# Optimization experiments

Measured on AMD Instinct MI355X. Metric: run time of the kernel, lower is better.

## Reference

```python
import jax, jax.numpy as jnp
import numpy as np

B, S, D, H = 2, 2048, 1024, 16
HD = D // H  # head_dim = 64

def setup_inputs() -> dict:
    key = jax.random.key(0)
    ks = jax.random.split(key, 5)
    scale = 1.0 / np.sqrt(D)
    x = jax.random.normal(ks[0], (B, S, D), dtype=jnp.float32)
    Wq = jax.random.normal(ks[1], (D, D), dtype=jnp.float32) * scale
    Wk = jax.random.normal(ks[2], (D, D), dtype=jnp.float32) * scale
    Wv = jax.random.normal(ks[3], (D, D), dtype=jnp.float32) * scale
    Wf = jax.random.normal(ks[4], (D, D), dtype=jnp.float32) * scale
    z = jnp.zeros((D,), dtype=jnp.float32)
    return {"x": x, "Wq": Wq, "bq": z, "Wk": Wk, "bk": z, "Wv": Wv, "bv": z, "Wf": Wf, "bf": z}

def reference(x, Wq, bq, Wk, bk, Wv, bv, Wf, bf):
    # Linear layers follow torch convention: y = x @ W.T + b
    def split_heads(t):  # [B,S,D] -> [B,H,S,HD]
        return t.reshape(B, S, H, HD).transpose(0, 2, 1, 3)
    q = split_heads(x @ Wq.T + bq)
    k = split_heads(x @ Wk.T + bk)
    v = split_heads(x @ Wv.T + bv)
    scores = jnp.einsum('bhqd,bhkd->bhqk', q, k) / jnp.sqrt(jnp.float32(HD))
    causal = jnp.tril(jnp.ones((S, S), dtype=bool))  # [S,S]
    scores = jnp.where(causal[None, None], scores, -jnp.inf)
    attn = jax.nn.softmax(scores, axis=-1)
    out = jnp.einsum('bhqk,bhkd->bhqd', attn, v)
    out = out.transpose(0, 2, 1, 3).reshape(B, S, D)
    return out @ Wf.T + bf
```

## Files before the change

kernel.cpp:

```cpp
#include <hip/hip_runtime.h>
#include <stdint.h>

#define B_  2
#define S_  2048
#define D_  1024
#define H_  16
#define HD_ 64
#define M_  (B_*S_)

typedef __bf16 bf16x8 __attribute__((ext_vector_type(8)));
typedef float  f32x4  __attribute__((ext_vector_type(4)));

typedef const __attribute__((address_space(1))) void* gas_ptr;
typedef __attribute__((address_space(3))) void* las_ptr;

__device__ __forceinline__ uint16_t f32_to_bf16(float f) {
  uint32_t u = __float_as_uint(f);
  u += 0x7FFFu + ((u >> 16) & 1u);
  return (uint16_t)(u >> 16);
}

__device__ __forceinline__ void g2l16(const uint16_t* g, uint16_t* l) {
  __builtin_amdgcn_global_load_lds((gas_ptr)g, (las_ptr)l, 16, 0, 0);
}

__device__ __forceinline__ int swz_src(int s) {
  return (s >> 2) * D_ + (((s & 3) ^ ((s >> 3) & 3)) * 8);
}

__global__ void cast_all(const float* __restrict__ x,
                         const float* __restrict__ wq, const float* __restrict__ wk,
                         const float* __restrict__ wv, const float* __restrict__ wf,
                         uint16_t* __restrict__ xb,
                         uint16_t* __restrict__ wqb, uint16_t* __restrict__ wkb,
                         uint16_t* __restrict__ wvb, uint16_t* __restrict__ wfb) {
  const int X4 = M_ * D_ / 4;
  const int W4 = D_ * D_ / 4;
  int i = blockIdx.x * 256 + threadIdx.x;
  const float* src; uint16_t* dst; int off;
  if (i < X4) { src = x; dst = xb; off = i; }
  else {
    int j = i - X4;
    int w = j >> 18;
    off = j & (W4 - 1);
    src = (w == 0) ? wq : (w == 1) ? wk : (w == 2) ? wv : wf;
    dst = (w == 0) ? wqb : (w == 1) ? wkb : (w == 2) ? wvb : wfb;
  }
  float4 v = ((const float4*)src)[off];
  ushort4 o;
  o.x = f32_to_bf16(v.x); o.y = f32_to_bf16(v.y);
  o.z = f32_to_bf16(v.z); o.w = f32_to_bf16(v.w);
  ((ushort4*)dst)[off] = o;
}

__device__ __forceinline__ void gemm_tile_128_swz(
    const uint16_t* __restrict__ A, const uint16_t* __restrict__ B,
    int am0, int bn0, uint16_t* As, uint16_t* Bs, f32x4 (&acc)[4][4])
{
  const int tid  = threadIdx.x;
  const int wave = tid >> 6;
  const int lane = tid & 63;
  const int quad = lane >> 4;
  const int l16  = lane & 15;
  const int wm = (wave >> 1) * 64;
  const int wn = (wave & 1) * 64;
  const int sw = quad ^ ((l16 >> 1) & 3);

  #pragma unroll
  for (int i = 0; i < 4; ++i)
    #pragma unroll
    for (int j = 0; j < 4; ++j)
      #pragma unroll
      for (int e = 0; e < 4; ++e)
        acc[i][j][e] = 0.f;

  const int s0 = wave * 64 + lane;
  const int s1 = s0 + 256;
  uint16_t* lA0 = As + (size_t)(wave * 64) * 8;
  uint16_t* lA1 = As + (size_t)(256 + wave * 64) * 8;
  uint16_t* lB0 = Bs + (size_t)(wave * 64) * 8;
  uint16_t* lB1 = Bs + (size_t)(256 + wave * 64) * 8;
  const uint16_t* gA0 = A + (size_t)am0 * D_ + swz_src(s0);
  const uint16_t* gA1 = A + (size_t)am0 * D_ + swz_src(s1);
  const uint16_t* gB0 = B + (size_t)bn0 * D_ + swz_src(s0);
  const uint16_t* gB1 = B + (size_t)bn0 * D_ + swz_src(s1);

  for (int k0 = 0; k0 < D_; k0 += 32) {
    g2l16(gA0 + k0, lA0);
    g2l16(gA1 + k0, lA1);
    g2l16(gB0 + k0, lB0);
    g2l16(gB1 + k0, lB1);
    __syncthreads();
    bf16x8 af[4], bfr[4];
    #pragma unroll
    for (int mt = 0; mt < 4; ++mt)
      af[mt] = *(const bf16x8*)(As + ((wm + mt * 16 + l16) * 4 + sw) * 8);
    #pragma unroll
    for (int nt = 0; nt < 4; ++nt)
      bfr[nt] = *(const bf16x8*)(Bs + ((wn + nt * 16 + l16) * 4 + sw) * 8);
    #pragma unroll
    for (int mt = 0; mt < 4; ++mt)
      #pragma unroll
      for (int nt = 0; nt < 4; ++nt)
        acc[mt][nt] = __builtin_amdgcn_mfma_f32_16x16x32_bf16(
            af[mt], bfr[nt], acc[mt][nt], 0, 0, 0);
    __syncthreads();
  }
}

__global__ __launch_bounds__(256)
void qkv_gemm(const uint16_t* __restrict__ xb,
              const uint16_t* __restrict__ wqb, const uint16_t* __restrict__ wkb,
              const uint16_t* __restrict__ wvb,
              const float* __restrict__ bqv, const float* __restrict__ bkv,
              const float* __restrict__ bvv,
              uint16_t* __restrict__ qout, uint16_t* __restrict__ kout,
              uint16_t* __restrict__ vtout)
{
  __shared__ __align__(16) uint16_t As[128 * 32];
  __shared__ __align__(16) uint16_t Bs[128 * 32];
  const int wsel = blockIdx.x >> 3;
  const int nsel = blockIdx.x & 7;
  const int mtile = blockIdx.y;
  const int lane = threadIdx.x & 63, wave = threadIdx.x >> 6;
  const int quad = lane >> 4, l16 = lane & 15;
  const int wm = (wave >> 1) * 64, wn = (wave & 1) * 64;

  const uint16_t *Ap, *Bp;
  int m0e, n0e;
  if (wsel < 2) {
    Ap = xb; Bp = (wsel == 0) ? wqb : wkb;
    m0e = mtile * 128; n0e = nsel * 128;
  } else {
    Ap = wvb; Bp = xb;
    m0e = nsel * 128; n0e = mtile * 128;
  }
  f32x4 acc[4][4];
  gemm_tile_128_swz(Ap, Bp, m0e, n0e, As, Bs, acc);

  if (wsel < 2) {
    const float* bias = (wsel == 0) ? bqv : bkv;
    uint16_t* outp = (wsel == 0) ? qout : kout;
    const float scl = (wsel == 0) ? 0.18033688f : 1.0f;
    #pragma unroll
    for (int nt = 0; nt < 4; ++nt) {
      const int n = n0e + wn + nt * 16 + l16;
      const int h = n >> 6, hd = n & 63;
      const float bia = bias[n];
      #pragma unroll
      for (int mt = 0; mt < 4; ++mt) {
        #pragma unroll
        for (int r = 0; r < 4; ++r) {
          const int m = m0e + wm + mt * 16 + quad * 4 + r;
          const int bb = m >> 11, s = m & (S_ - 1);
          outp[(((size_t)(bb * H_ + h)) * S_ + s) * HD_ + hd] =
              f32_to_bf16((acc[mt][nt][r] + bia) * scl);
        }
      }
    }
  } else {
    #pragma unroll
    for (int mt = 0; mt < 4; ++mt) {
      #pragma unroll
      for (int r = 0; r < 4; ++r) {
        const int m = m0e + wm + mt * 16 + quad * 4 + r;
        const int h = m >> 6, hd = m & 63;
        const float bia = bvv[m];
        #pragma unroll
        for (int nt = 0; nt < 4; ++nt) {
          const int n = n0e + wn + nt * 16 + l16;
          const int bb = n >> 11, s = n & (S_ - 1);
          vtout[(((size_t)(bb * H_ + h)) * HD_ + hd) * S_ + s] =
              f32_to_bf16(acc[mt][nt][r] + bia);
        }
      }
    }
  }
}

__global__ __launch_bounds__(256)
void flash_attn(const uint16_t* __restrict__ qb, const uint16_t* __restrict__ kb,
                const uint16_t* __restrict__ vtb, uint16_t* __restrict__ ao)
{
  __shared__ __align__(16) uint16_t ks[2][64 * 32];
  __shared__ __align__(16) uint16_t vs[2][64 * 32];
  __shared__ __align__(16) uint16_t p_lds[4][16][72];

  const int bh = blockIdx.x;
  const int qt = (int)(gridDim.y - 1u - blockIdx.y);
  const int wave = threadIdx.x >> 6, lane = threadIdx.x & 63;
  const int quad = lane >> 4, l16 = lane & 15;
  const int sw = quad ^ ((l16 >> 1) & 3);
  const int q0 = qt * 64;

  const uint16_t* Q  = qb  + (size_t)bh * S_ * HD_;
  const uint16_t* Kp = kb  + (size_t)bh * S_ * HD_;
  const uint16_t* Vt = vtb + (size_t)bh * HD_ * S_;

  const int qrow = q0 + wave * 16;
  bf16x8 aq0 = *(const bf16x8*)(Q + (size_t)(qrow + l16) * HD_ + quad * 8);
  bf16x8 aq1 = *(const bf16x8*)(Q + (size_t)(qrow + l16) * HD_ + 32 + quad * 8);

  const int srow = lane >> 2;
  const int schk = (lane & 3) ^ ((lane >> 3) & 3);
  const uint16_t* sb[4]; uint16_t* sdst[4]; int sstep[4];
  #pragma unroll
  for (int j = 0; j < 4; ++j) {
    const int g = wave * 4 + j;
    if (g < 8) {
      const int c = (g >> 2) & 1, rb = g & 3;
      sdst[j] = &ks[c][rb * 512];
      sb[j] = Kp + (size_t)(rb * 16 + srow) * HD_ + c * 32 + schk * 8;
      sstep[j] = 64 * HD_;
    } else {
      const int gg = g - 8, c = (gg >> 2) & 1, rb = gg & 3;
      sdst[j] = &vs[c][rb * 512];
      sb[j] = Vt + (size_t)(rb * 16 + srow) * S_ + c * 32 + schk * 8;
      sstep[j] = 64;
    }
  }

  float lpart[4];
  f32x4 o[4];
  #pragma unroll
  for (int r = 0; r < 4; ++r) lpart[r] = 0.f;
  #pragma unroll
  for (int t = 0; t < 4; ++t)
    #pragma unroll
    for (int e = 0; e < 4; ++e) o[t][e] = 0.f;

  const int rowid = qrow + quad * 4;

  for (int kt = 0; kt <= qt; ++kt) {
    const int kbase = kt * 64;
    const bool diag = (kt == qt);

    #pragma unroll
    for (int j = 0; j < 4; ++j) {
      g2l16(sb[j], sdst[j]);
      sb[j] += sstep[j];
    }
    __syncthreads();

    bf16x8 kf0[4], kf1[4];
    #pragma unroll
    for (int nt = 0; nt < 4; ++nt) {
      kf0[nt] = *(const bf16x8*)(&ks[0][((nt * 16 + l16) * 4 + sw) * 8]);
      kf1[nt] = *(const bf16x8*)(&ks[1][((nt * 16 + l16) * 4 + sw) * 8]);
    }
    f32x4 sacc[4];
    #pragma unroll
    for (int nt = 0; nt < 4; ++nt) {
      #pragma unroll
      for (int e = 0; e < 4; ++e) sacc[nt][e] = 0.f;
      sacc[nt] = __builtin_amdgcn_mfma_f32_16x16x32_bf16(aq0, kf0[nt], sacc[nt], 0, 0, 0);
      sacc[nt] = __builtin_amdgcn_mfma_f32_16x16x32_bf16(aq1, kf1[nt], sacc[nt], 0, 0, 0);
    }

    bf16x8 vf0[4], vf1[4];
    #pragma unroll
    for (int t = 0; t < 4; ++t) {
      vf0[t] = *(const bf16x8*)(&vs[0][((t * 16 + l16) * 4 + sw) * 8]);
      vf1[t] = *(const bf16x8*)(&vs[1][((t * 16 + l16) * 4 + sw) * 8]);
    }

    #pragma unroll
    for (int nt = 0; nt < 4; ++nt) {
      const int kkc = kbase + nt * 16 + l16;
      #pragma unroll
      for (int r = 0; r < 4; ++r) {
        float p = __builtin_amdgcn_exp2f(sacc[nt][r]);
        if (diag && (kkc > rowid + r)) p = 0.f;
        lpart[r] += p;
        p_lds[wave][quad * 4 + r][nt * 16 + l16] = f32_to_bf16(p);
      }
    }

    bf16x8 ap0 = *(const bf16x8*)(&p_lds[wave][l16][quad * 8]);
    bf16x8 ap1 = *(const bf16x8*)(&p_lds[wave][l16][32 + quad * 8]);
    #pragma unroll
    for (int t = 0; t < 4; ++t) {
      o[t] = __builtin_amdgcn_mfma_f32_16x16x32_bf16(ap0, vf0[t], o[t], 0, 0, 0);
      o[t] = __builtin_amdgcn_mfma_f32_16x16x32_bf16(ap1, vf1[t], o[t], 0, 0, 0);
    }
    __syncthreads();
  }

  #pragma unroll
  for (int r = 0; r < 4; ++r) {
    lpart[r] += __shfl_xor(lpart[r], 1, 64);
    lpart[r] += __shfl_xor(lpart[r], 2, 64);
    lpart[r] += __shfl_xor(lpart[r], 4, 64);
    lpart[r] += __shfl_xor(lpart[r], 8, 64);
  }
  const int bb = bh >> 4, h = bh & 15;
  #pragma unroll
  for (int t = 0; t < 4; ++t) {
    #pragma unroll
    for (int r = 0; r < 4; ++r) {
      const float ov = o[t][r] / lpart[r];
      ao[((size_t)(bb * S_ + rowid + r)) * D_ + h * HD_ + t * 16 + l16] =
          f32_to_bf16(ov);
    }
  }
}

__global__ __launch_bounds__(256)
void out_gemm(const uint16_t* __restrict__ ab, const uint16_t* __restrict__ wfb,
              const float* __restrict__ bfv, float* __restrict__ out)
{
  __shared__ __align__(16) uint16_t As[64 * 32];
  __shared__ __align__(16) uint16_t Bs[128 * 32];
  const int m0 = blockIdx.y * 64;
  const int n0 = blockIdx.x * 128;
  const int lane = threadIdx.x & 63, wave = threadIdx.x >> 6;
  const int quad = lane >> 4, l16 = lane & 15;
  const int wm = (wave >> 1) * 32, wn = (wave & 1) * 64;
  const int sw = quad ^ ((l16 >> 1) & 3);

  f32x4 acc[2][4];
  #pragma unroll
  for (int i = 0; i < 2; ++i)
    #pragma unroll
    for (int j = 0; j < 4; ++j)
      #pragma unroll
      for (int e = 0; e < 4; ++e)
        acc[i][j][e] = 0.f;

  const int sA  = wave * 64 + lane;
  const int sB1 = sA + 256;
  uint16_t* lA  = As + (size_t)(wave * 64) * 8;
  uint16_t* lB0 = Bs + (size_t)(wave * 64) * 8;
  uint16_t* lB1 = Bs + (size_t)(256 + wave * 64) * 8;
  const uint16_t* gA  = ab  + (size_t)m0 * D_ + swz_src(sA);
  const uint16_t* gB0 = wfb + (size_t)n0 * D_ + swz_src(sA);
  const uint16_t* gB1 = wfb + (size_t)n0 * D_ + swz_src(sB1);

  for (int k0 = 0; k0 < D_; k0 += 32) {
    g2l16(gA  + k0, lA);
    g2l16(gB0 + k0, lB0);
    g2l16(gB1 + k0, lB1);
    __syncthreads();
    bf16x8 af[2], bfr[4];
    #pragma unroll
    for (int mt = 0; mt < 2; ++mt)
      af[mt] = *(const bf16x8*)(As + ((wm + mt * 16 + l16) * 4 + sw) * 8);
    #pragma unroll
    for (int nt = 0; nt < 4; ++nt)
      bfr[nt] = *(const bf16x8*)(Bs + ((wn + nt * 16 + l16) * 4 + sw) * 8);
    #pragma unroll
    for (int mt = 0; mt < 2; ++mt)
      #pragma unroll
      for (int nt = 0; nt < 4; ++nt)
        acc[mt][nt] = __builtin_amdgcn_mfma_f32_16x16x32_bf16(
            af[mt], bfr[nt], acc[mt][nt], 0, 0, 0);
    __syncthreads();
  }

  #pragma unroll
  for (int nt = 0; nt < 4; ++nt) {
    const int n = n0 + wn + nt * 16 + l16;
    const float bia = bfv[n];
    #pragma unroll
    for (int mt = 0; mt < 2; ++mt) {
      #pragma unroll
      for (int r = 0; r < 4; ++r) {
        const int m = m0 + wm + mt * 16 + quad * 4 + r;
        out[(size_t)m * D_ + n] = acc[mt][nt][r] + bia;
      }
    }
  }
}

extern "C" void kernel_launch(void* const* d_in, const int* in_sizes, int n_in,
                              void* d_out, int out_size, void* d_ws, size_t ws_size,
                              hipStream_t stream) {
  (void)in_sizes; (void)n_in; (void)out_size; (void)ws_size;
  const float* x  = (const float*)d_in[0];
  const float* Wq = (const float*)d_in[1];
  const float* bq = (const float*)d_in[2];
  const float* Wk = (const float*)d_in[3];
  const float* bk = (const float*)d_in[4];
  const float* Wv = (const float*)d_in[5];
  const float* bv = (const float*)d_in[6];
  const float* Wf = (const float*)d_in[7];
  const float* bf = (const float*)d_in[8];
  float* out = (float*)d_out;

  uint16_t* ws = (uint16_t*)d_ws;
  uint16_t* xb   = ws;
  uint16_t* wqb  = xb  + (size_t)M_ * D_;
  uint16_t* wkb  = wqb + (size_t)D_ * D_;
  uint16_t* wvb  = wkb + (size_t)D_ * D_;
  uint16_t* wfb  = wvb + (size_t)D_ * D_;
  uint16_t* qbuf = wfb + (size_t)D_ * D_;
  uint16_t* kbuf = qbuf + (size_t)M_ * D_;
  uint16_t* vtb  = kbuf + (size_t)M_ * D_;
  uint16_t* aob  = vtb  + (size_t)M_ * D_;

  const int CAST_BLOCKS = (M_ * D_ / 4 + 4 * (D_ * D_ / 4)) / 256;
  cast_all<<<CAST_BLOCKS, 256, 0, stream>>>(x, Wq, Wk, Wv, Wf,
                                            xb, wqb, wkb, wvb, wfb);

  qkv_gemm<<<dim3(24, 32), 256, 0, stream>>>(xb, wqb, wkb, wvb, bq, bk, bv,
                                             qbuf, kbuf, vtb);
  flash_attn<<<dim3(32, 32), 256, 0, stream>>>(qbuf, kbuf, vtb, aob);
  out_gemm<<<dim3(8, 64), 256, 0, stream>>>(aob, wfb, bf, out);
}
```

Baseline: 190.5 us.

## Double-buffer LDS staging in GEMMs and flash attention, use truncating bf16 cast

Gives the QKV GEMM, output GEMM and flash-attention K/V tiles two LDS buffers. The next tile's global-to-LDS load is issued right after the barrier, so it overlaps with the MFMA work on the current tile, and the second barrier per iteration is removed. The probability values written to LDS in attention now use a truncating bf16 conversion instead of round-to-nearest, which saves a few ALU ops per element at some cost in accuracy. LDS use per block roughly doubles, which may lower occupancy. Correctness of the single barrier depends on global_load_lds completing before the next barrier, and this relies on the compiler inserting a vmcnt wait.

```diff
diff --git a/kernel.cpp b/kernel.cpp
--- a/kernel.cpp
+++ b/kernel.cpp
@@ -18,6 +18,10 @@
   uint32_t u = __float_as_uint(f);
   u += 0x7FFFu + ((u >> 16) & 1u);
   return (uint16_t)(u >> 16);
+}
+
+__device__ __forceinline__ uint16_t f32_to_bf16_rtz(float f) {
+  return (uint16_t)(__float_as_uint(f) >> 16);
 }
 
 __device__ __forceinline__ void g2l16(const uint16_t* g, uint16_t* l) {
@@ -53,9 +57,10 @@
   ((ushort4*)dst)[off] = o;
 }
 
-__device__ __forceinline__ void gemm_tile_128_swz(
+__device__ __forceinline__ void gemm_tile_128_dbuf(
     const uint16_t* __restrict__ A, const uint16_t* __restrict__ B,
-    int am0, int bn0, uint16_t* As, uint16_t* Bs, f32x4 (&acc)[4][4])
+    int am0, int bn0, uint16_t (*As)[128 * 32], uint16_t (*Bs)[128 * 32],
+    f32x4 (&acc)[4][4])
 {
   const int tid  = threadIdx.x;
   const int wave = tid >> 6;
@@ -76,35 +81,40 @@
 
   const int s0 = wave * 64 + lane;
   const int s1 = s0 + 256;
-  uint16_t* lA0 = As + (size_t)(wave * 64) * 8;
-  uint16_t* lA1 = As + (size_t)(256 + wave * 64) * 8;
-  uint16_t* lB0 = Bs + (size_t)(wave * 64) * 8;
-  uint16_t* lB1 = Bs + (size_t)(256 + wave * 64) * 8;
-  const uint16_t* gA0 = A + (size_t)am0 * D_ + swz_src(s0);
-  const uint16_t* gA1 = A + (size_t)am0 * D_ + swz_src(s1);
-  const uint16_t* gB0 = B + (size_t)bn0 * D_ + swz_src(s0);
-  const uint16_t* gB1 = B + (size_t)bn0 * D_ + swz_src(s1);
-
-  for (int k0 = 0; k0 < D_; k0 += 32) {
-    g2l16(gA0 + k0, lA0);
-    g2l16(gA1 + k0, lA1);
-    g2l16(gB0 + k0, lB0);
-    g2l16(gB1 + k0, lB1);
+  const int so0 = swz_src(s0), so1 = swz_src(s1);
+  const int d0 = (wave * 64) * 8;
+  const int d1 = (256 + wave * 64) * 8;
+  const uint16_t* gA0 = A + (size_t)am0 * D_ + so0;
+  const uint16_t* gA1 = A + (size_t)am0 * D_ + so1;
+  const uint16_t* gB0 = B + (size_t)bn0 * D_ + so0;
+  const uint16_t* gB1 = B + (size_t)bn0 * D_ + so1;
+
+  auto stage = [&](int buf, int k0) {
+    g2l16(gA0 + k0, As[buf] + d0);
+    g2l16(gA1 + k0, As[buf] + d1);
+    g2l16(gB0 + k0, Bs[buf] + d0);
+    g2l16(gB1 + k0, Bs[buf] + d1);
+  };
+
+  stage(0, 0);
+  for (int it = 0; it < 32; ++it) {
     __syncthreads();
+    if (it + 1 < 32) stage((it + 1) & 1, (it + 1) * 32);
+    const uint16_t* as = As[it & 1];
+    const uint16_t* bs = Bs[it & 1];
     bf16x8 af[4], bfr[4];
     #pragma unroll
     for (int mt = 0; mt < 4; ++mt)
-      af[mt] = *(const bf16x8*)(As + ((wm + mt * 16 + l16) * 4 + sw) * 8);
+      af[mt] = *(const bf16x8*)(as + ((wm + mt * 16 + l16) * 4 + sw) * 8);
     #pragma unroll
     for (int nt = 0; nt < 4; ++nt)
-      bfr[nt] = *(const bf16x8*)(Bs + ((wn + nt * 16 + l16) * 4 + sw) * 8);
+      bfr[nt] = *(const bf16x8*)(bs + ((wn + nt * 16 + l16) * 4 + sw) * 8);
     #pragma unroll
     for (int mt = 0; mt < 4; ++mt)
       #pragma unroll
       for (int nt = 0; nt < 4; ++nt)
         acc[mt][nt] = __builtin_amdgcn_mfma_f32_16x16x32_bf16(
             af[mt], bfr[nt], acc[mt][nt], 0, 0, 0);
-    __syncthreads();
   }
 }
 
@@ -117,8 +127,8 @@
               uint16_t* __restrict__ qout, uint16_t* __restrict__ kout,
               uint16_t* __restrict__ vtout)
 {
-  __shared__ __align__(16) uint16_t As[128 * 32];
-  __shared__ __align__(16) uint16_t Bs[128 * 32];
+  __shared__ __align__(16) uint16_t As[2][128 * 32];
+  __shared__ __align__(16) uint16_t Bs[2][128 * 32];
   const int wsel = blockIdx.x >> 3;
   const int nsel = blockIdx.x & 7;
   const int mtile = blockIdx.y;
@@ -136,7 +146,7 @@
     m0e = nsel * 128; n0e = mtile * 128;
   }
   f32x4 acc[4][4];
-  gemm_tile_128_swz(Ap, Bp, m0e, n0e, As, Bs, acc);
+  gemm_tile_128_dbuf(Ap, Bp, m0e, n0e, As, Bs, acc);
 
   if (wsel < 2) {
     const float* bias = (wsel == 0) ? bqv : bkv;
@@ -182,8 +192,8 @@
 void flash_attn(const uint16_t* __restrict__ qb, const uint16_t* __restrict__ kb,
                 const uint16_t* __restrict__ vtb, uint16_t* __restrict__ ao)
 {
-  __shared__ __align__(16) uint16_t ks[2][64 * 32];
-  __shared__ __align__(16) uint16_t vs[2][64 * 32];
+  __shared__ __align__(16) uint16_t ks[2][2][64 * 32];
+  __shared__ __align__(16) uint16_t vs[2][2][64 * 32];
   __shared__ __align__(16) uint16_t p_lds[4][16][72];
 
   const int bh = blockIdx.x;
@@ -203,22 +213,31 @@
 
   const int srow = lane >> 2;
   const int schk = (lane & 3) ^ ((lane >> 3) & 3);
-  const uint16_t* sb[4]; uint16_t* sdst[4]; int sstep[4];
+  const uint16_t* sb[4]; int sstep[4], g_c[4], g_rb[4]; bool g_isk[4];
   #pragma unroll
   for (int j = 0; j < 4; ++j) {
     const int g = wave * 4 + j;
     if (g < 8) {
-      const int c = (g >> 2) & 1, rb = g & 3;
-      sdst[j] = &ks[c][rb * 512];
-      sb[j] = Kp + (size_t)(rb * 16 + srow) * HD_ + c * 32 + schk * 8;
+      g_isk[j] = true; g_c[j] = (g >> 2) & 1; g_rb[j] = g & 3;
+      sb[j] = Kp + (size_t)(g_rb[j] * 16 + srow) * HD_ + g_c[j] * 32 + schk * 8;
       sstep[j] = 64 * HD_;
     } else {
-      const int gg = g - 8, c = (gg >> 2) & 1, rb = gg & 3;
-      sdst[j] = &vs[c][rb * 512];
-      sb[j] = Vt + (size_t)(rb * 16 + srow) * S_ + c * 32 + schk * 8;
+      const int gg = g - 8;
+      g_isk[j] = false; g_c[j] = (gg >> 2) & 1; g_rb[j] = gg & 3;
+      sb[j] = Vt + (size_t)(g_rb[j] * 16 + srow) * S_ + g_c[j] * 32 + schk * 8;
       sstep[j] = 64;
     }
   }
+
+  auto stage = [&](int buf) {
+    #pragma unroll
+    for (int j = 0; j < 4; ++j) {
+      uint16_t* d = g_isk[j] ? &ks[buf][g_c[j]][g_rb[j] * 512]
+                             : &vs[buf][g_c[j]][g_rb[j] * 512];
+      g2l16(sb[j], d);
+      sb[j] += sstep[j];
+    }
+  };
 
   float lpart[4];
   f32x4 o[4];
@@ -231,22 +250,21 @@
 
   const int rowid = qrow + quad * 4;
 
+  stage(0);
   for (int kt = 0; kt <= qt; ++kt) {
+    const int cur = kt & 1;
     const int kbase = kt * 64;
     const bool diag = (kt == qt);
 
-    #pragma unroll
-    for (int j = 0; j < 4; ++j) {
-      g2l16(sb[j], sdst[j]);
-      sb[j] += sstep[j];
-    }
     __syncthreads();
+    if (kt < qt) stage(cur ^ 1);
 
     bf16x8 kf0[4], kf1[4];
     #pragma unroll
     for (int nt = 0; nt < 4; ++nt) {
-      kf0[nt] = *(const bf16x8*)(&ks[0][((nt * 16 + l16) * 4 + sw) * 8]);
-      kf1[nt] = *(const bf16x8*)(&ks[1][((nt * 16 + l16) * 4 + sw) * 8]);
+      const int ro = ((nt * 16 + l16) * 4 + sw) * 8;
+      kf0[nt] = *(const bf16x8*)(&ks[cur][0][ro]);
+      kf1[nt] = *(const bf16x8*)(&ks[cur][1][ro]);
     }
     f32x4 sacc[4];
     #pragma unroll
@@ -260,8 +278,9 @@
     bf16x8 vf0[4], vf1[4];
     #pragma unroll
     for (int t = 0; t < 4; ++t) {
-      vf0[t] = *(const bf16x8*)(&vs[0][((t * 16 + l16) * 4 + sw) * 8]);
-      vf1[t] = *(const bf16x8*)(&vs[1][((t * 16 + l16) * 4 + sw) * 8]);
+      const int ro = ((t * 16 + l16) * 4 + sw) * 8;
+      vf0[t] = *(const bf16x8*)(&vs[cur][0][ro]);
+      vf1[t] = *(const bf16x8*)(&vs[cur][1][ro]);
     }
 
     #pragma unroll
@@ -272,7 +291,7 @@
         float p = __builtin_amdgcn_exp2f(sacc[nt][r]);
         if (diag && (kkc > rowid + r)) p = 0.f;
         lpart[r] += p;
-        p_lds[wave][quad * 4 + r][nt * 16 + l16] = f32_to_bf16(p);
+        p_lds[wave][quad * 4 + r][nt * 16 + l16] = f32_to_bf16_rtz(p);
       }
     }
 
@@ -283,7 +302,6 @@
       o[t] = __builtin_amdgcn_mfma_f32_16x16x32_bf16(ap0, vf0[t], o[t], 0, 0, 0);
       o[t] = __builtin_amdgcn_mfma_f32_16x16x32_bf16(ap1, vf1[t], o[t], 0, 0, 0);
     }
-    __syncthreads();
   }
 
   #pragma unroll
@@ -309,8 +327,8 @@
 void out_gemm(const uint16_t* __restrict__ ab, const uint16_t* __restrict__ wfb,
               const float* __restrict__ bfv, float* __restrict__ out)
 {
-  __shared__ __align__(16) uint16_t As[64 * 32];
-  __shared__ __align__(16) uint16_t Bs[128 * 32];
+  __shared__ __align__(16) uint16_t As[2][64 * 32];
+  __shared__ __align__(16) uint16_t Bs[2][128 * 32];
   const int m0 = blockIdx.y * 64;
   const int n0 = blockIdx.x * 128;
   const int lane = threadIdx.x & 63, wave = threadIdx.x >> 6;
@@ -329,32 +347,38 @@
 
   const int sA  = wave * 64 + lane;
   const int sB1 = sA + 256;
-  uint16_t* lA  = As + (size_t)(wave * 64) * 8;
-  uint16_t* lB0 = Bs + (size_t)(wave * 64) * 8;
-  uint16_t* lB1 = Bs + (size_t)(256 + wave * 64) * 8;
-  const uint16_t* gA  = ab  + (size_t)m0 * D_ + swz_src(sA);
-  const uint16_t* gB0 = wfb + (size_t)n0 * D_ + swz_src(sA);
-  const uint16_t* gB1 = wfb + (size_t)n0 * D_ + swz_src(sB1);
-
-  for (int k0 = 0; k0 < D_; k0 += 32) {
-    g2l16(gA  + k0, lA);
-    g2l16(gB0 + k0, lB0);
-    g2l16(gB1 + k0, lB1);
+  const int soA = swz_src(sA), soB1 = swz_src(sB1);
+  const int d0 = (wave * 64) * 8;
+  const int d1 = (256 + wave * 64) * 8;
+  const uint16_t* gA  = ab  + (size_t)m0 * D_ + soA;
+  const uint16_t* gB0 = wfb + (size_t)n0 * D_ + soA;
+  const uint16_t* gB1 = wfb + (size_t)n0 * D_ + soB1;
+
+  auto stage = [&](int buf, int k0) {
+    g2l16(gA  + k0, As[buf] + d0);
+    g2l16(gB0 + k0, Bs[buf] + d0);
+    g2l16(gB1 + k0, Bs[buf] + d1);
+  };
+
+  stage(0, 0);
+  for (int it = 0; it < 32; ++it) {
     __syncthreads();
+    if (it + 1 < 32) stage((it + 1) & 1, (it + 1) * 32);
+    const uint16_t* as = As[it & 1];
+    const uint16_t* bs = Bs[it & 1];
     bf16x8 af[2], bfr[4];
     #pragma unroll
     for (int mt = 0; mt < 2; ++mt)
-      af[mt] = *(const bf16x8*)(As + ((wm + mt * 16 + l16) * 4 + sw) * 8);
+      af[mt] = *(const bf16x8*)(as + ((wm + mt * 16 + l16) * 4 + sw) * 8);
     #pragma unroll
     for (int nt = 0; nt < 4; ++nt)
-      bfr[nt] = *(const bf16x8*)(Bs + ((wn + nt * 16 + l16) * 4 + sw) * 8);
+      bfr[nt] = *(const bf16x8*)(bs + ((wn + nt * 16 + l16) * 4 + sw) * 8);
     #pragma unroll
     for (int mt = 0; mt < 2; ++mt)
       #pragma unroll
       for (int nt = 0; nt < 4; ++nt)
         acc[mt][nt] = __builtin_amdgcn_mfma_f32_16x16x32_bf16(
             af[mt], bfr[nt], acc[mt][nt], 0, 0, 0);
-    __syncthreads();
   }
 
   #pragma unroll
```

Result: no change. 194.1 us (+1.8%).
